# Optimization experiments

Hardware: AMD Instinct MI355X
Metric: run time of the kernel (lower is better)

The kernel has to match this reference:

```python
import jax, jax.numpy as jnp
import numpy as np

NUM_ITERS = 3

def squash(t, axis):
    # scale = |t|^2/(1+|t|^2); out = scale * t / |t|
    sn = jnp.sum(t * t, axis=axis, keepdims=True)
    return (sn / (1.0 + sn)) * t / jnp.sqrt(sn)


def setup_inputs() -> dict:
    key = jax.random.key(0)
    k1, k2, k3, k4 = jax.random.split(key, 4)
    B = 128
    inputs = jax.random.normal(k1, (B, 256, 20, 20), dtype=jnp.float32)
    conv_w = jax.random.normal(k2, (8, 32, 256, 9, 9), dtype=jnp.float32) * 0.05
    conv_b = jax.random.normal(k3, (8, 32), dtype=jnp.float32) * 0.05
    route_weights = jax.random.normal(k4, (10, 1152, 8, 16), dtype=jnp.float32)
    return {"inputs": inputs, "conv_w": conv_w, "conv_b": conv_b,
            "route_weights": route_weights}


def reference(inputs, conv_w, conv_b, route_weights):
    B = inputs.shape[0]
    K, O, Cin, kh, kw = conv_w.shape          # 8 capsules, 32 out-chans each
    # --- primary capsules: 8 parallel convs fused into one grouped-output conv ---
    w = conv_w.reshape(K * O, Cin, kh, kw)
    out = jax.lax.conv_general_dilated(
        inputs, w, window_strides=(2, 2), padding='VALID',
        dimension_numbers=('NCHW', 'OIHW', 'NCHW'))  # [B, K*O, 6, 6]
    out = out + conv_b.reshape(K * O)[None, :, None, None]
    H = out.shape[-1]
    x = out.reshape(B, K, O * H * H).transpose(0, 2, 1)  # [B, 1152, 8]
    x = squash(x, axis=2)
    # --- routing layer ---
    # prediction_vectors: x[None,:,:,None,:] @ W[:,None,:,:,:] -> [10,B,1152,1,16]
    pred = jnp.einsum('bri,crio->cbro', x, route_weights)[:, :, :, None, :]
    logits = jnp.zeros_like(pred)
    v = None
    for i in range(NUM_ITERS):
        # routing_softmax(dim=2): softmax over the routes axis (faithful to source)
        c = jax.nn.softmax(logits, axis=2)
        s = jnp.sum(c * pred, axis=2, keepdims=True)  # [10,B,1,1,16]
        v = squash(s, axis=1)                          # squash default dim=1 (batch) -- faithful
        if i != NUM_ITERS - 1:
            logits = logits + jnp.sum(pred * v, axis=-1, keepdims=True)
    # [10,B,1,1,16] -> squeeze -> [10,B,16] -> permute(1,0,2) -> [B,10,16]
    return jnp.squeeze(v).transpose(1, 0, 2)
```

## Files before the change

### kernel.cpp

```cpp
#include <hip/hip_runtime.h>
#include <math.h>

typedef _Float16 f16;
typedef _Float16 f16x8 __attribute__((ext_vector_type(8)));
typedef float f32x4 __attribute__((ext_vector_type(4)));
typedef float f32x8 __attribute__((ext_vector_type(8)));

#define AS1 __attribute__((address_space(1)))
#define AS3 __attribute__((address_space(3)))

__device__ __forceinline__ void gld_lds16(const f16* g, f16* l) {
#if defined(__has_builtin) && __has_builtin(__builtin_amdgcn_global_load_lds)
    __builtin_amdgcn_global_load_lds((const AS1 void*)g, (AS3 void*)l, 16, 0, 0);
#else
    *(uint4*)l = *(const uint4*)g;
#endif
}

__global__ __launch_bounds__(256) void transpose_input(
    const float* __restrict__ inp, f16* __restrict__ out)
{
    const int b = blockIdx.x, c0 = blockIdx.y * 32, p0 = blockIdx.z * 32;
    const int tx = threadIdx.x, ty = threadIdx.y;
    __shared__ float t[32][33];
#pragma unroll
    for (int j = 0; j < 4; ++j) {
        int c = ty + j * 8, p = p0 + tx;
        if (p < 400) t[c][tx] = inp[((size_t)b * 256 + c0 + c) * 400 + p];
    }
    __syncthreads();
#pragma unroll
    for (int j = 0; j < 4; ++j) {
        int p = p0 + ty + j * 8;
        if (p < 400) out[((size_t)b * 400 + p) * 256 + c0 + tx] = (f16)t[tx][ty + j * 8];
    }
}

__global__ __launch_bounds__(256) void permute_w(
    const float* __restrict__ cw, f16* __restrict__ w_t)
{
    const int n = blockIdx.x, t = threadIdx.x;
    __shared__ f16 buf[81 * 258];
    const float* src = cw + (size_t)n * 20736;
    for (int i = t; i < 20736; i += 256) {
        int cin = i / 81, p = i - cin * 81;
        buf[p * 258 + cin] = (f16)src[i];
    }
    __syncthreads();
    f16* dst = w_t + (size_t)n * 20736;
    for (int j = t; j < 20736; j += 256) {
        int p = j >> 8, cin = j & 255;
        dst[j] = buf[p * 258 + cin];
    }
}

#define SPLITK 18
#define CITER 36
__global__ __launch_bounds__(256) void conv_mfma(
    const f16* __restrict__ in_t,
    const f16* __restrict__ w_t,
    f16* __restrict__ part)
{
    __shared__ f16 As[2][128 * 32];
    __shared__ f16 Bs[2][128 * 32];
    const int tid = threadIdx.x;
    const int lane = tid & 63, wave = tid >> 6;
    const int wm = wave >> 1, wn = wave & 1;
    const int m0 = blockIdx.x * 128, n0 = blockIdx.y * 128;
    const int kz = blockIdx.z;

    int srcA[2], srcB[2];
#pragma unroll
    for (int i = 0; i < 2; ++i) {
        int pairp = i * 32 + (tid >> 3);
        int chunk8 = (tid & 7) ^ (pairp & 7);
        int e = chunk8 >> 2, q4 = chunk8 & 3;
        int m = m0 + pairp * 2 + e;
        int b = m / 36, hw = m - b * 36;
        int ho = hw / 6, wo = hw - ho * 6;
        srcA[i] = ((b * 20 + 2 * ho) * 20 + 2 * wo) * 256 + q4 * 8;
        int n = n0 + pairp * 2 + e;
        srcB[i] = n * 20736 + q4 * 8;
    }

    f32x4 acc[4][4] = {};
    const int row = lane & 15, quad = lane >> 4;
    const int kc_base = kz * CITER;

    {
        int kc = kc_base;
        int p = kc >> 3, cq = kc & 7;
        int kh = p / 9, kw = p - kh * 9;
        int koffA = (kh * 20 + kw) * 256 + cq * 32;
        int koffB = kc * 32;
#pragma unroll
        for (int i = 0; i < 2; ++i) {
            gld_lds16(in_t + srcA[i] + koffA, &As[0][i * 2048 + tid * 8]);
            gld_lds16(w_t + srcB[i] + koffB, &Bs[0][i * 2048 + tid * 8]);
        }
    }

    for (int it = 0; it < CITER; ++it) {
        const int cur = it & 1;
        __syncthreads();
        if (it + 1 < CITER) {
            int kc = kc_base + it + 1;
            int p = kc >> 3, cq = kc & 7;
            int kh = p / 9, kw = p - kh * 9;
            int koffA = (kh * 20 + kw) * 256 + cq * 32;
            int koffB = kc * 32;
#pragma unroll
            for (int i = 0; i < 2; ++i) {
                gld_lds16(in_t + srcA[i] + koffA, &As[cur ^ 1][i * 2048 + tid * 8]);
                gld_lds16(w_t + srcB[i] + koffB, &Bs[cur ^ 1][i * 2048 + tid * 8]);
            }
        }
        f16x8 af[4], bf[4];
#pragma unroll
        for (int mt = 0; mt < 4; ++mt) {
            int m = wm * 64 + mt * 16 + row;
            int ph8 = (((m & 1) << 2) + quad) ^ ((m >> 1) & 7);
            af[mt] = *(const f16x8*)(&As[cur][(m >> 1) * 64 + ph8 * 8]);
        }
#pragma unroll
        for (int nt = 0; nt < 4; ++nt) {
            int n = wn * 64 + nt * 16 + row;
            int ph8 = (((n & 1) << 2) + quad) ^ ((n >> 1) & 7);
            bf[nt] = *(const f16x8*)(&Bs[cur][(n >> 1) * 64 + ph8 * 8]);
        }
#pragma unroll
        for (int mt = 0; mt < 4; ++mt)
#pragma unroll
            for (int nt = 0; nt < 4; ++nt)
                acc[mt][nt] = __builtin_amdgcn_mfma_f32_16x16x32_f16(
                    af[mt], bf[nt], acc[mt][nt], 0, 0, 0);
    }

    const int col = lane & 15, qr = (lane >> 4) * 4;
    f16* pb = part + (size_t)kz * 4608 * 256;
#pragma unroll
    for (int mt = 0; mt < 4; ++mt)
#pragma unroll
        for (int rg = 0; rg < 4; ++rg) {
            int m = m0 + wm * 64 + mt * 16 + qr + rg;
#pragma unroll
            for (int nt = 0; nt < 4; ++nt) {
                int n = n0 + wn * 64 + nt * 16 + col;
                pb[(size_t)m * 256 + n] = (f16)acc[mt][nt][rg];
            }
        }
}

__global__ __launch_bounds__(256) void combine_squash(
    const f16* __restrict__ part, const float* __restrict__ bias,
    float* __restrict__ x)
{
    int idx = blockIdx.x * 256 + threadIdx.x;
    int m = idx >> 5, o = idx & 31;
    int b = m / 36, hw = m - b * 36;
    float val[8];
#pragma unroll
    for (int k = 0; k < 8; ++k) val[k] = bias[k * 32 + o];
#pragma unroll
    for (int s = 0; s < SPLITK; ++s) {
        const f16* p = part + ((size_t)s * 4608 + m) * 256 + o;
#pragma unroll
        for (int k = 0; k < 8; ++k) val[k] += (float)p[k * 32];
    }
    float sn = 0.f;
#pragma unroll
    for (int k = 0; k < 8; ++k) sn += val[k] * val[k];
    float scale = sqrtf(sn) / (1.f + sn);
    int r = o * 36 + hw;
    float* xp = x + ((size_t)b * 1152 + r) * 8;
#pragma unroll
    for (int k = 0; k < 8; ++k) xp[k] = val[k] * scale;
}

__global__ __launch_bounds__(256) void pred_s0(
    const float* __restrict__ x, const float* __restrict__ rw,
    f16* __restrict__ pred, float* __restrict__ s0)
{
    const int c = blockIdx.x, r0 = blockIdx.y * 32, b0 = blockIdx.z * 32;
    const int tid = threadIdx.x;
    const int o = tid & 15, rp = tid >> 4;
    const int r = r0 + rp * 2;

    __shared__ float s_sh[32 * 16];
    s_sh[tid] = 0.f; s_sh[tid + 256] = 0.f;

    float W0[8], W1[8];
    const float* wb = rw + ((size_t)(c * 1152 + r) * 8) * 16 + o;
#pragma unroll
    for (int k = 0; k < 8; ++k) { W0[k] = wb[k * 16]; W1[k] = wb[128 + k * 16]; }
    __syncthreads();

    for (int bb = 0; bb < 32; ++bb) {
        const int b = b0 + bb;
        const float4* xp = (const float4*)(x + ((size_t)b * 1152 + r) * 8);
        float4 xa = xp[0], xb = xp[1], xc = xp[2], xd = xp[3];
        float p0 = xa.x * W0[0] + xa.y * W0[1] + xa.z * W0[2] + xa.w * W0[3]
                 + xb.x * W0[4] + xb.y * W0[5] + xb.z * W0[6] + xb.w * W0[7];
        float p1 = xc.x * W1[0] + xc.y * W1[1] + xc.z * W1[2] + xc.w * W1[3]
                 + xd.x * W1[4] + xd.y * W1[5] + xd.z * W1[6] + xd.w * W1[7];
        f16* pb = pred + ((size_t)(c * 128 + b) * 1152 + r) * 16 + o;
        pb[0]  = (f16)p0;
        pb[16] = (f16)p1;
        float ps = p0 + p1;
        ps += __shfl_xor(ps, 16);
        ps += __shfl_xor(ps, 32);
        if ((tid & 63) < 16) atomicAdd(&s_sh[bb * 16 + o], ps);
    }
    __syncthreads();
    for (int i = tid; i < 512; i += 256) {
        int bb = i >> 4, oo = i & 15;
        atomicAdd(&s0[((size_t)c * 128 + b0 + bb) * 16 + oo], s_sh[i]);
    }
}

__global__ __launch_bounds__(256) void route_f16(
    const f16* __restrict__ pred, const float* __restrict__ s_in,
    const float* __restrict__ z_in, const float* __restrict__ a_in,
    float* __restrict__ a_out, float* __restrict__ s_out, float* __restrict__ z_out)
{
    const int c = blockIdx.x, b = blockIdx.y, tid = threadIdx.x;
    const size_t base = (size_t)(c * 128 + b) * 1152;

    __shared__ float vs[16];
    __shared__ float mat[128][17];
    __shared__ float red[256][16];
    __shared__ float red2[16][16];
    __shared__ float zred[256];
    __shared__ float zpart[16];

    {
        if (tid < 128) {
            float zin = z_in ? 1.f / z_in[c * 128 + tid] : (1.f / 1152.f);
            const float* sp = s_in + (size_t)(c * 128 + tid) * 16;
#pragma unroll
            for (int o = 0; o < 16; ++o) mat[tid][o] = sp[o] * zin;
        }
        __syncthreads();
        if (tid < 16) {
            float sn = 0.f;
            for (int i = 0; i < 128; ++i) { float q = mat[i][tid]; sn += q * q; }
            vs[tid] = mat[b][tid] * sqrtf(sn) / (1.f + sn);
        }
        __syncthreads();
    }

    float sacc[16];
#pragma unroll
    for (int o = 0; o < 16; ++o) sacc[o] = 0.f;
    float zacc = 0.f;

    for (int r = tid; r < 1152; r += 256) {
        const f16x8* pp = (const f16x8*)(pred + (base + r) * 16);
        f32x8 q0 = __builtin_convertvector(pp[0], f32x8);
        f32x8 q1 = __builtin_convertvector(pp[1], f32x8);
        float contrib = 0.f;
#pragma unroll
        for (int j = 0; j < 8; ++j) contrib += q0[j] * vs[j] + q1[j] * vs[j + 8];
        float an = contrib + (a_in ? a_in[base + r] : 0.f);
        if (a_out) a_out[base + r] = an;
        float e = __expf(an);
#pragma unroll
        for (int j = 0; j < 8; ++j) { sacc[j] += e * q0[j]; sacc[j + 8] += e * q1[j]; }
        zacc += e;
    }

#pragma unroll
    for (int o = 0; o < 16; ++o) red[tid][o] = sacc[o];
    zred[tid] = zacc;
    __syncthreads();
    {
        const int o = tid & 15, seg = tid >> 4;
        float t = 0.f;
#pragma unroll
        for (int j = 0; j < 16; ++j) t += red[seg * 16 + j][o];
        red2[seg][o] = t;
        if (tid < 16) {
            float tz = 0.f;
#pragma unroll
            for (int j = 0; j < 16; ++j) tz += zred[tid * 16 + j];
            zpart[tid] = tz;
        }
    }
    __syncthreads();
    if (tid < 16) {
        float t = 0.f;
#pragma unroll
        for (int seg = 0; seg < 16; ++seg) t += red2[seg][tid];
        s_out[(size_t)(c * 128 + b) * 16 + tid] = t;
    } else if (tid == 16) {
        float tz = 0.f;
#pragma unroll
        for (int j = 0; j < 16; ++j) tz += zpart[j];
        z_out[c * 128 + b] = tz;
    }
}

__global__ __launch_bounds__(128) void squash_final(
    const float* __restrict__ s, const float* __restrict__ z,
    float* __restrict__ out)
{
    const int c = blockIdx.x, b = threadIdx.x;
    float sv[16];
    const float* sp = s + ((size_t)c * 128 + b) * 16;
    float zin = 1.f / z[c * 128 + b];
#pragma unroll
    for (int o = 0; o < 16; ++o) sv[o] = sp[o] * zin;
    __shared__ float m[16][129];
#pragma unroll
    for (int o = 0; o < 16; ++o) m[o][b] = sv[o] * sv[o];
    __syncthreads();
    __shared__ float sn[16];
    if (b < 16) {
        float t = 0.f;
        for (int i = 0; i < 128; ++i) t += m[b][i];
        sn[b] = t;
    }
    __syncthreads();
#pragma unroll
    for (int o = 0; o < 16; ++o) {
        float scale = sqrtf(sn[o]) / (1.f + sn[o]);
        out[((size_t)b * 10 + c) * 16 + o] = sv[o] * scale;
    }
}

extern "C" void kernel_launch(void* const* d_in, const int* in_sizes, int n_in,
                              void* d_out, int out_size, void* d_ws, size_t ws_size,
                              hipStream_t stream)
{
    (void)in_sizes; (void)n_in; (void)out_size; (void)ws_size;
    const float* inp = (const float*)d_in[0];
    const float* cw  = (const float*)d_in[1];
    const float* cb  = (const float*)d_in[2];
    const float* rw  = (const float*)d_in[3];
    float* out = (float*)d_out;

    char* ws = (char*)d_ws;
    f16*   part = (f16*)(ws);
    f16*   pred = (f16*)(ws);
    float* x    = (float*)(ws + 47185920);
    float* a    = (float*)(ws + 51904512);
    float* sA   = (float*)(ws + 57802752);
    float* zA   = (float*)(ws + 57884672);
    float* sB   = (float*)(ws + 57889792);
    float* zB   = (float*)(ws + 57971712);
    f16*   in_t = (f16*)(ws + 57976832);
    f16*   w_t  = (f16*)(ws + 84191232);

    transpose_input<<<dim3(128, 8, 13), dim3(32, 8), 0, stream>>>(inp, in_t);
    permute_w<<<256, 256, 0, stream>>>(cw, w_t);
    conv_mfma<<<dim3(36, 2, SPLITK), 256, 0, stream>>>(in_t, w_t, part);
    combine_squash<<<576, 256, 0, stream>>>(part, cb, x);

    hipMemsetAsync(sA, 0, 81920, stream);
    pred_s0<<<dim3(10, 36, 4), 256, 0, stream>>>(x, rw, pred, sA);

    route_f16<<<dim3(10, 128), 256, 0, stream>>>(pred, sA, nullptr, nullptr,
                                                 a, sB, zB);
    route_f16<<<dim3(10, 128), 256, 0, stream>>>(pred, sB, zB, a,
                                                 nullptr, sA, zA);
    squash_final<<<10, 128, 0, stream>>>(sA, zA, out);
}
```

Before: 280.5 us.

## Enlarge conv GEMM tile, vectorize input transpose and pred_s0 stores

The conv MFMA kernel now uses a 256x128 block tile with 8x4 accumulators per wave and moves from 18 to 27 split-K slices. That raises reuse per LDS load and changes the partial-sum footprint, so the workspace offsets are shifted to fit. The input transpose now handles 64 pixels per block and writes 8-wide f16 vectors, and pred_s0 stages x in shared memory and writes 4-wide f16 vectors per thread. The cost is higher register and LDS pressure in the conv kernel, more partial sums for the combine step to read, and extra block-wide syncs per batch iteration in pred_s0.

```diff
diff --git a/kernel.cpp b/kernel.cpp
--- a/kernel.cpp
+++ b/kernel.cpp
@@ -3,6 +3,7 @@
 
 typedef _Float16 f16;
 typedef _Float16 f16x8 __attribute__((ext_vector_type(8)));
+typedef _Float16 f16x4 __attribute__((ext_vector_type(4)));
 typedef float f32x4 __attribute__((ext_vector_type(4)));
 typedef float f32x8 __attribute__((ext_vector_type(8)));
 
@@ -20,19 +21,30 @@
 __global__ __launch_bounds__(256) void transpose_input(
     const float* __restrict__ inp, f16* __restrict__ out)
 {
-    const int b = blockIdx.x, c0 = blockIdx.y * 32, p0 = blockIdx.z * 32;
-    const int tx = threadIdx.x, ty = threadIdx.y;
-    __shared__ float t[32][33];
-#pragma unroll
-    for (int j = 0; j < 4; ++j) {
-        int c = ty + j * 8, p = p0 + tx;
-        if (p < 400) t[c][tx] = inp[((size_t)b * 256 + c0 + c) * 400 + p];
-    }
-    __syncthreads();
-#pragma unroll
-    for (int j = 0; j < 4; ++j) {
-        int p = p0 + ty + j * 8;
-        if (p < 400) out[((size_t)b * 400 + p) * 256 + c0 + tx] = (f16)t[tx][ty + j * 8];
+    const int b = blockIdx.x, c0 = blockIdx.y * 32, p0 = blockIdx.z * 64;
+    const int tid = threadIdx.x;
+    __shared__ float t[32][65];
+    {
+        const int p_l = tid & 63, c_l = tid >> 6;
+        const int p = p0 + p_l;
+        if (p < 400) {
+#pragma unroll
+            for (int j = 0; j < 8; ++j) {
+                int c = c_l + j * 4;
+                t[c][p_l] = inp[((size_t)b * 256 + c0 + c) * 400 + p];
+            }
+        }
+    }
+    __syncthreads();
+    {
+        const int p_w = tid >> 2, og = tid & 3;
+        const int p = p0 + p_w;
+        if (p < 400) {
+            f16x8 v;
+#pragma unroll
+            for (int e = 0; e < 8; ++e) v[e] = (f16)t[og * 8 + e][p_w];
+            *(f16x8*)(out + ((size_t)b * 400 + p) * 256 + c0 + og * 8) = v;
+        }
     }
 }
 
@@ -54,24 +66,24 @@
     }
 }
 
-#define SPLITK 18
-#define CITER 36
+#define SPLITK 27
+#define CITER 24
 __global__ __launch_bounds__(256) void conv_mfma(
     const f16* __restrict__ in_t,
     const f16* __restrict__ w_t,
     f16* __restrict__ part)
 {
-    __shared__ f16 As[2][128 * 32];
+    __shared__ f16 As[2][256 * 32];
     __shared__ f16 Bs[2][128 * 32];
     const int tid = threadIdx.x;
     const int lane = tid & 63, wave = tid >> 6;
     const int wm = wave >> 1, wn = wave & 1;
-    const int m0 = blockIdx.x * 128, n0 = blockIdx.y * 128;
+    const int m0 = blockIdx.x * 256, n0 = blockIdx.y * 128;
     const int kz = blockIdx.z;
 
-    int srcA[2], srcB[2];
-#pragma unroll
-    for (int i = 0; i < 2; ++i) {
+    int srcA[4], srcB[2];
+#pragma unroll
+    for (int i = 0; i < 4; ++i) {
         int pairp = i * 32 + (tid >> 3);
         int chunk8 = (tid & 7) ^ (pairp & 7);
         int e = chunk8 >> 2, q4 = chunk8 & 3;
@@ -79,11 +91,17 @@
         int b = m / 36, hw = m - b * 36;
         int ho = hw / 6, wo = hw - ho * 6;
         srcA[i] = ((b * 20 + 2 * ho) * 20 + 2 * wo) * 256 + q4 * 8;
+    }
+#pragma unroll
+    for (int i = 0; i < 2; ++i) {
+        int pairp = i * 32 + (tid >> 3);
+        int chunk8 = (tid & 7) ^ (pairp & 7);
+        int e = chunk8 >> 2, q4 = chunk8 & 3;
         int n = n0 + pairp * 2 + e;
         srcB[i] = n * 20736 + q4 * 8;
     }
 
-    f32x4 acc[4][4] = {};
+    f32x4 acc[8][4] = {};
     const int row = lane & 15, quad = lane >> 4;
     const int kc_base = kz * CITER;
 
@@ -94,10 +112,11 @@
         int koffA = (kh * 20 + kw) * 256 + cq * 32;
         int koffB = kc * 32;
 #pragma unroll
-        for (int i = 0; i < 2; ++i) {
+        for (int i = 0; i < 4; ++i)
             gld_lds16(in_t + srcA[i] + koffA, &As[0][i * 2048 + tid * 8]);
+#pragma unroll
+        for (int i = 0; i < 2; ++i)
             gld_lds16(w_t + srcB[i] + koffB, &Bs[0][i * 2048 + tid * 8]);
-        }
     }
 
     for (int it = 0; it < CITER; ++it) {
@@ -110,15 +129,16 @@
             int koffA = (kh * 20 + kw) * 256 + cq * 32;
             int koffB = kc * 32;
 #pragma unroll
-            for (int i = 0; i < 2; ++i) {
+            for (int i = 0; i < 4; ++i)
                 gld_lds16(in_t + srcA[i] + koffA, &As[cur ^ 1][i * 2048 + tid * 8]);
+#pragma unroll
+            for (int i = 0; i < 2; ++i)
                 gld_lds16(w_t + srcB[i] + koffB, &Bs[cur ^ 1][i * 2048 + tid * 8]);
-            }
-        }
-        f16x8 af[4], bf[4];
-#pragma unroll
-        for (int mt = 0; mt < 4; ++mt) {
-            int m = wm * 64 + mt * 16 + row;
+        }
+        f16x8 af[8], bf[4];
+#pragma unroll
+        for (int mt = 0; mt < 8; ++mt) {
+            int m = wm * 128 + mt * 16 + row;
             int ph8 = (((m & 1) << 2) + quad) ^ ((m >> 1) & 7);
             af[mt] = *(const f16x8*)(&As[cur][(m >> 1) * 64 + ph8 * 8]);
         }
@@ -129,7 +149,7 @@
             bf[nt] = *(const f16x8*)(&Bs[cur][(n >> 1) * 64 + ph8 * 8]);
         }
 #pragma unroll
-        for (int mt = 0; mt < 4; ++mt)
+        for (int mt = 0; mt < 8; ++mt)
 #pragma unroll
             for (int nt = 0; nt < 4; ++nt)
                 acc[mt][nt] = __builtin_amdgcn_mfma_f32_16x16x32_f16(
@@ -139,10 +159,10 @@
     const int col = lane & 15, qr = (lane >> 4) * 4;
     f16* pb = part + (size_t)kz * 4608 * 256;
 #pragma unroll
-    for (int mt = 0; mt < 4; ++mt)
+    for (int mt = 0; mt < 8; ++mt)
 #pragma unroll
         for (int rg = 0; rg < 4; ++rg) {
-            int m = m0 + wm * 64 + mt * 16 + qr + rg;
+            int m = m0 + wm * 128 + mt * 16 + qr + rg;
 #pragma unroll
             for (int nt = 0; nt < 4; ++nt) {
                 int n = n0 + wn * 64 + nt * 16 + col;
@@ -181,41 +201,62 @@
     const float* __restrict__ x, const float* __restrict__ rw,
     f16* __restrict__ pred, float* __restrict__ s0)
 {
-    const int c = blockIdx.x, r0 = blockIdx.y * 32, b0 = blockIdx.z * 32;
+    const int c = blockIdx.x, r0 = blockIdx.y * 64, b0 = blockIdx.z * 32;
     const int tid = threadIdx.x;
-    const int o = tid & 15, rp = tid >> 4;
-    const int r = r0 + rp * 2;
+    const int og = tid & 3, rl = tid >> 2;
+    const int r = r0 + rl;
 
     __shared__ float s_sh[32 * 16];
+    __shared__ float xs[64][8];
     s_sh[tid] = 0.f; s_sh[tid + 256] = 0.f;
 
-    float W0[8], W1[8];
-    const float* wb = rw + ((size_t)(c * 1152 + r) * 8) * 16 + o;
-#pragma unroll
-    for (int k = 0; k < 8; ++k) { W0[k] = wb[k * 16]; W1[k] = wb[128 + k * 16]; }
-    __syncthreads();
+    float W[8][4];
+    {
+        const float* wb = rw + ((size_t)(c * 1152 + r) * 8) * 16 + og * 4;
+#pragma unroll
+        for (int k = 0; k < 8; ++k) {
+            float4 w4 = *(const float4*)(wb + k * 16);
+            W[k][0] = w4.x; W[k][1] = w4.y; W[k][2] = w4.z; W[k][3] = w4.w;
+        }
+    }
 
     for (int bb = 0; bb < 32; ++bb) {
         const int b = b0 + bb;
-        const float4* xp = (const float4*)(x + ((size_t)b * 1152 + r) * 8);
-        float4 xa = xp[0], xb = xp[1], xc = xp[2], xd = xp[3];
-        float p0 = xa.x * W0[0] + xa.y * W0[1] + xa.z * W0[2] + xa.w * W0[3]
-                 + xb.x * W0[4] + xb.y * W0[5] + xb.z * W0[6] + xb.w * W0[7];
-        float p1 = xc.x * W1[0] + xc.y * W1[1] + xc.z * W1[2] + xc.w * W1[3]
-                 + xd.x * W1[4] + xd.y * W1[5] + xd.z * W1[6] + xd.w * W1[7];
-        f16* pb = pred + ((size_t)(c * 128 + b) * 1152 + r) * 16 + o;
-        pb[0]  = (f16)p0;
-        pb[16] = (f16)p1;
-        float ps = p0 + p1;
-        ps += __shfl_xor(ps, 16);
-        ps += __shfl_xor(ps, 32);
-        if ((tid & 63) < 16) atomicAdd(&s_sh[bb * 16 + o], ps);
-    }
-    __syncthreads();
-    for (int i = tid; i < 512; i += 256) {
-        int bb = i >> 4, oo = i & 15;
-        atomicAdd(&s0[((size_t)c * 128 + b0 + bb) * 16 + oo], s_sh[i]);
-    }
+        __syncthreads();
+        if (tid < 128)
+            *(float4*)&xs[tid >> 1][(tid & 1) * 4] =
+                *(const float4*)(x + ((size_t)b * 1152 + r0 + (tid >> 1)) * 8 + (tid & 1) * 4);
+        __syncthreads();
+
+        float p[4];
+        {
+            const float* xr = xs[rl];
+#pragma unroll
+            for (int j = 0; j < 4; ++j) p[j] = xr[0] * W[0][j];
+#pragma unroll
+            for (int k = 1; k < 8; ++k)
+#pragma unroll
+                for (int j = 0; j < 4; ++j) p[j] += xr[k] * W[k][j];
+        }
+        {
+            f16x4 pv;
+#pragma unroll
+            for (int j = 0; j < 4; ++j) pv[j] = (f16)p[j];
+            *(f16x4*)(pred + ((size_t)(c * 128 + b) * 1152 + r) * 16 + og * 4) = pv;
+        }
+#pragma unroll
+        for (int j = 0; j < 4; ++j) {
+            float v = p[j];
+            v += __shfl_xor(v, 4);
+            v += __shfl_xor(v, 8);
+            v += __shfl_xor(v, 16);
+            v += __shfl_xor(v, 32);
+            if ((tid & 63) < 4) atomicAdd(&s_sh[bb * 16 + og * 4 + j], v);
+        }
+    }
+    __syncthreads();
+    for (int i = tid; i < 512; i += 256)
+        atomicAdd(&s0[((size_t)c * 128 + b0 + (i >> 4)) * 16 + (i & 15)], s_sh[i]);
 }
 
 __global__ __launch_bounds__(256) void route_f16(
@@ -342,22 +383,22 @@
     char* ws = (char*)d_ws;
     f16*   part = (f16*)(ws);
     f16*   pred = (f16*)(ws);
-    float* x    = (float*)(ws + 47185920);
-    float* a    = (float*)(ws + 51904512);
-    float* sA   = (float*)(ws + 57802752);
-    float* zA   = (float*)(ws + 57884672);
-    float* sB   = (float*)(ws + 57889792);
-    float* zB   = (float*)(ws + 57971712);
-    f16*   in_t = (f16*)(ws + 57976832);
-    f16*   w_t  = (f16*)(ws + 84191232);
-
-    transpose_input<<<dim3(128, 8, 13), dim3(32, 8), 0, stream>>>(inp, in_t);
+    float* x    = (float*)(ws + 63700992);
+    float* a    = (float*)(ws + 68419584);
+    float* sA   = (float*)(ws + 74317824);
+    float* zA   = (float*)(ws + 74399744);
+    float* sB   = (float*)(ws + 74404864);
+    float* zB   = (float*)(ws + 74486784);
+    f16*   in_t = (f16*)(ws + 74491904);
+    f16*   w_t  = (f16*)(ws + 100706304);
+
+    transpose_input<<<dim3(128, 8, 7), 256, 0, stream>>>(inp, in_t);
     permute_w<<<256, 256, 0, stream>>>(cw, w_t);
-    conv_mfma<<<dim3(36, 2, SPLITK), 256, 0, stream>>>(in_t, w_t, part);
+    conv_mfma<<<dim3(18, 2, SPLITK), 256, 0, stream>>>(in_t, w_t, part);
     combine_squash<<<576, 256, 0, stream>>>(part, cb, x);
 
     hipMemsetAsync(sA, 0, 81920, stream);
-    pred_s0<<<dim3(10, 36, 4), 256, 0, stream>>>(x, rw, pred, sA);
+    pred_s0<<<dim3(10, 18, 4), 256, 0, stream>>>(x, rw, pred, sA);
 
     route_f16<<<dim3(10, 128), 256, 0, stream>>>(pred, sA, nullptr, nullptr,
                                                  a, sB, zB);
```

Measured after the change: 289.6 us. 1.03x slower.
